# Kernel tuning notes

Hardware: AMD Instinct MI355X
Metric: run time of the kernel (lower is better)

The kernel has to match this reference:

```python
import jax, jax.numpy as jnp
import numpy as np

N, S, P, F = 128, 32, 16, 256   # agents, samples, processes, encoder dim
H, NH = 4, 128                  # heads, n_hidden (is_concat=False -> n_hidden=out_features)
SLOPE = 0.2


def setup_inputs() -> dict:
    key = jax.random.key(0)
    k1, k2, k3, k4 = jax.random.split(key, 4)
    h = jax.random.normal(k1, (N, S, P, F), dtype=jnp.float32)
    W_l = jax.random.normal(k2, (F, H * NH), dtype=jnp.float32) / np.float32(np.sqrt(F))
    W_r = jax.random.normal(k3, (F, H * NH), dtype=jnp.float32) / np.float32(np.sqrt(F))
    attn_w = jax.random.normal(k4, (2 * NH,), dtype=jnp.float32) / np.float32(np.sqrt(2 * NH))
    return {"h": h, "W_l": W_l, "W_r": W_r, "attn_w": attn_w}


def reference(h, W_l, W_r, attn_w):
    n, s, p, f = h.shape
    hp = jnp.transpose(h, (1, 2, 0, 3))                 # [S,P,N,F]
    g_l = (hp @ W_l).reshape(s, p, n, H, NH)            # [S,P,N,H,NH]
    g_r = (hp @ W_r).reshape(s, p, n, H, NH)
    # attn(concat(gl[j], gr[i])) == <gl[j], a_l> + <gr[i], a_r>
    a_l, a_r = attn_w[:NH], attn_w[NH:]
    score_l = jnp.einsum('spnhf,f->spnh', g_l, a_l)     # contributes along j
    score_r = jnp.einsum('spnhf,f->spnh', g_r, a_r)     # contributes along i
    e = score_r[:, :, :, None, :] + score_l[:, :, None, :, :]   # [S,P,i,j,H]
    e = jnp.where(e >= 0, e, SLOPE * e)                 # LeakyReLU
    diag = jnp.eye(n, dtype=bool)[None, None, :, :, None]
    e = jnp.where(diag, -jnp.inf, e)                    # mask self-attention
    a = jax.nn.softmax(e, axis=3)                       # softmax over j
    out = jnp.einsum('spijh,spjhf->spihf', a, g_r)      # [S,P,N,H,NH]
    out = out.mean(axis=3)                              # is_concat=False -> mean over heads
    out = jnp.transpose(out, (2, 0, 1, 3))              # [N,S,P,NH]
    return out, a
```

## Files before the change

### kernel.cpp

```cpp
#include <hip/hip_runtime.h>
#include <hip/hip_bf16.h>

#define DI __device__ __forceinline__

namespace {
constexpr int N_ = 128, S_ = 32, P_ = 16, F_ = 256, H_ = 4, NH_ = 128;
constexpr int SP_ = S_ * P_;
constexpr int ROWS_ = N_ * SP_;
constexpr int GC_ = H_ * NH_;
constexpr float SLOPE_ = 0.2f;
constexpr int OUT_ELEMS = N_ * SP_ * NH_;
}

DI float lrelu(float x) { return x >= 0.f ? x : SLOPE_ * x; }

DI unsigned short f2h(float x) {
    _Float16 h = (_Float16)x;
    return __builtin_bit_cast(unsigned short, h);
}
DI float h2f(unsigned short b) {
    return (float)__builtin_bit_cast(_Float16, b);
}

typedef _Float16 f16x8 __attribute__((ext_vector_type(8)));
typedef float    f32x4 __attribute__((ext_vector_type(4)));

DI f32x4 mfma16h(uint4 a, uint4 b, f32x4 c) {
    return __builtin_amdgcn_mfma_f32_16x16x32_f16(
        __builtin_bit_cast(f16x8, a), __builtin_bit_cast(f16x8, b), c, 0, 0, 0);
}

__global__ __launch_bounds__(256) void prep_kernel(
    const float* __restrict__ Wl, const float* __restrict__ Wr,
    const float* __restrict__ aw, float* __restrict__ wls, float* __restrict__ wrs) {
    int t = blockIdx.x * 256 + threadIdx.x;
    int which = t >> 10;
    int f = (t & 1023) >> 2;
    int h = t & 3;
    const float* W = which ? Wr : Wl;
    const float* a = aw + which * NH_;
    const float* wrow = W + (size_t)f * GC_ + h * NH_;
    float s = 0.f;
    for (int k = 0; k < NH_; ++k) s += wrow[k] * a[k];
    (which ? wrs : wls)[f * H_ + h] = s;
}

__global__ __launch_bounds__(256) void prep_bt(
    const float* __restrict__ Wr, unsigned short* __restrict__ bth,
    unsigned short* __restrict__ btl) {
    int t = blockIdx.x * 256 + threadIdx.x;
    int col = t >> 5, k0 = (t & 31) * 8;
    union { unsigned short us[8]; uint4 v; } ph, pl;
#pragma unroll
    for (int e = 0; e < 8; ++e) {
        float v = Wr[(size_t)(k0 + e) * GC_ + col] * 256.0f;
        unsigned short hi = f2h(v);
        ph.us[e] = hi;
        pl.us[e] = f2h(v - h2f(hi));
    }
    *(uint4*)&bth[col * F_ + k0] = ph.v;
    *(uint4*)&btl[col * F_ + k0] = pl.v;
}

__global__ __launch_bounds__(256) void score_kernel(
    const float* __restrict__ hm, const float* __restrict__ wls,
    const float* __restrict__ wrs, float* __restrict__ sl, float* __restrict__ sr) {
    int r = blockIdx.x * 256 + threadIdx.x;
    const float4* hr  = (const float4*)(hm + (size_t)r * F_);
    const float4* wl4 = (const float4*)wls;
    const float4* wr4 = (const float4*)wrs;
    float4 al = {0.f,0.f,0.f,0.f}, ar = {0.f,0.f,0.f,0.f};
    for (int f0 = 0; f0 < F_; f0 += 4) {
        float4 hv = hr[f0 >> 2];
        float hx[4] = {hv.x, hv.y, hv.z, hv.w};
#pragma unroll
        for (int u = 0; u < 4; ++u) {
            float4 wl = wl4[f0 + u], wr = wr4[f0 + u];
            al.x += hx[u] * wl.x; al.y += hx[u] * wl.y;
            al.z += hx[u] * wl.z; al.w += hx[u] * wl.w;
            ar.x += hx[u] * wr.x; ar.y += hx[u] * wr.y;
            ar.z += hx[u] * wr.z; ar.w += hx[u] * wr.w;
        }
    }
    int n = r >> 9, sp = r & 511;
    ((float4*)sl)[sp * N_ + n] = al;
    ((float4*)sr)[sp * N_ + n] = ar;
}

__global__ __launch_bounds__(512, 2) void gat_fused(
    const float* __restrict__ sl_g, const float* __restrict__ sr_g,
    const float* __restrict__ hm,
    const unsigned short* __restrict__ bth, const unsigned short* __restrict__ btl,
    float* __restrict__ a_out, float* __restrict__ out) {
    constexpr int PA = 40;
    __shared__ unsigned short Ah[2][128 * PA];
    __shared__ unsigned short Al[2][128 * PA];
    __shared__ unsigned short gt[128 * 128];
    __shared__ float4 sl4[N_], sr4[N_], mrow4[N_], invs4[N_];
    __shared__ float slh[H_][132];
    __shared__ float mx1[H_], mx2[H_];
    __shared__ int   id1[H_];

    int sp = blockIdx.x;
    int t = threadIdx.x;
    int w = t >> 6, l = t & 63;
    int ls = l & 15, kg = l >> 4;

    if (t < 128) {
        float4 v = ((const float4*)sl_g)[sp * N_ + t];
        sl4[t] = v;
        slh[0][t] = v.x; slh[1][t] = v.y; slh[2][t] = v.z; slh[3][t] = v.w;
    } else if (t < 256) {
        sr4[t - 128] = ((const float4*)sr_g)[sp * N_ + (t - 128)];
    }
    __syncthreads();

    if (t < H_) {
        float m1 = -1e30f; int i1 = 0;
        for (int j = 0; j < N_; ++j) {
            float v = ((const float*)&sl4[j])[t];
            if (v > m1) { m1 = v; i1 = j; }
        }
        float m2 = -1e30f;
        for (int j = 0; j < N_; ++j)
            if (j != i1) m2 = fmaxf(m2, ((const float*)&sl4[j])[t]);
        mx1[t] = m1; mx2[t] = m2; id1[t] = i1;
    }
    __syncthreads();

    int arow = t >> 2, akc = (t & 3) * 8;
    const float* abase = hm + ((size_t)arow * 512 + sp) * 256 + akc;
    float4 s0 = *(const float4*)(abase);
    float4 s1 = *(const float4*)(abase + 4);

    {
        int i = t & 127, h = t >> 7;
        float sri = ((const float*)&sr4[i])[h];
        float m = lrelu(sri + ((id1[h] == i) ? mx2[h] : mx1[h]));
        float sum = 0.f;
        for (int j = 0; j < N_; ++j) {
            float e = lrelu(sri + ((const float*)&sl4[j])[h]);
            float p = __expf(e - m);
            if (j != i) sum += p;
        }
        ((float*)&mrow4[i])[h] = m;
        ((float*)&invs4[i])[h] = 1.f / sum;
    }

    {
        float av[8] = {s0.x, s0.y, s0.z, s0.w, s1.x, s1.y, s1.z, s1.w};
        union { unsigned short us[8]; uint4 v; } ph, pl;
#pragma unroll
        for (int e = 0; e < 8; ++e) {
            unsigned short hi = f2h(av[e]);
            ph.us[e] = hi;
            pl.us[e] = f2h(av[e] - h2f(hi));
        }
        *(uint4*)&Ah[0][arow * PA + akc] = ph.v;
        *(uint4*)&Al[0][arow * PA + akc] = pl.v;
    }
    __syncthreads();

    f32x4 acc[8][4];
#pragma unroll
    for (int m = 0; m < 8; ++m)
#pragma unroll
        for (int n = 0; n < 4; ++n) acc[m][n] = (f32x4){0.f, 0.f, 0.f, 0.f};

    float4* a_base_g = (float4*)(a_out + (size_t)sp * 65536);
    int aj = t & 127, ib = t >> 7;
    float4 slv = sl4[aj];

    for (int step = 0; step < 8; ++step) {
        int cur = step & 1;
        float4 n0, n1;
        if (step < 7) {
            n0 = *(const float4*)(abase + (step + 1) * 32);
            n1 = *(const float4*)(abase + (step + 1) * 32 + 4);
        }
        int kglob = step * 32 + kg * 8;
        uint4 fbh[4], fbl[4];
#pragma unroll
        for (int n = 0; n < 4; ++n) {
            int c = n * 128 + w * 16 + ls;
            fbh[n] = *(const uint4*)&bth[(size_t)c * F_ + kglob];
            fbl[n] = *(const uint4*)&btl[(size_t)c * F_ + kglob];
        }
#pragma unroll
        for (int q = 0; q < 4; ++q) {
            int i = step * 16 + q * 4 + ib;
            float4 srv = sr4[i], m4 = mrow4[i], s4 = invs4[i];
            float4 p;
            p.x = __expf(lrelu(srv.x + slv.x) - m4.x) * s4.x;
            p.y = __expf(lrelu(srv.y + slv.y) - m4.y) * s4.y;
            p.z = __expf(lrelu(srv.z + slv.z) - m4.z) * s4.z;
            p.w = __expf(lrelu(srv.w + slv.w) - m4.w) * s4.w;
            if (aj == i) { p.x = 0.f; p.y = 0.f; p.z = 0.f; p.w = 0.f; }
            a_base_g[i * N_ + aj] = p;
        }
#pragma unroll
        for (int m = 0; m < 8; ++m) {
            int row = m * 16 + ls;
            uint4 fah = *(const uint4*)&Ah[cur][row * PA + kg * 8];
            uint4 fal = *(const uint4*)&Al[cur][row * PA + kg * 8];
#pragma unroll
            for (int n = 0; n < 4; ++n) {
                acc[m][n] = mfma16h(fah, fbh[n], acc[m][n]);
                acc[m][n] = mfma16h(fah, fbl[n], acc[m][n]);
                acc[m][n] = mfma16h(fal, fbh[n], acc[m][n]);
            }
        }
        if (step < 7) {
            float av[8] = {n0.x, n0.y, n0.z, n0.w, n1.x, n1.y, n1.z, n1.w};
            union { unsigned short us[8]; uint4 v; } ph, pl;
#pragma unroll
            for (int e = 0; e < 8; ++e) {
                unsigned short hi = f2h(av[e]);
                ph.us[e] = hi;
                pl.us[e] = f2h(av[e] - h2f(hi));
            }
            *(uint4*)&Ah[cur ^ 1][arow * PA + akc] = ph.v;
            *(uint4*)&Al[cur ^ 1][arow * PA + akc] = pl.v;
        }
        __syncthreads();
    }

    f32x4 aco[8];
#pragma unroll
    for (int n = 0; n < 8; ++n) aco[n] = (f32x4){0.f, 0.f, 0.f, 0.f};

    int i_my = w * 16 + ls;
    int fl   = w * 16 + ls;
    int swz  = (ls & 7) << 3;

    for (int h = 0; h < H_; ++h) {
        if (h) __syncthreads();

#pragma unroll
        for (int m = 0; m < 8; ++m) {
            int nodeb = m * 16 + kg * 4;
            union { unsigned short us[4]; uint2 v; } pk;
#pragma unroll
            for (int q = 0; q < 4; ++q) pk.us[q] = f2h(acc[m][h][q] * 0.00390625f);
            *(uint2*)&gt[fl * 128 + (nodeb ^ swz)] = pk.v;
        }
        __syncthreads();

        float sri = ((const float*)&sr4[i_my])[h];
        float mh  = ((const float*)&mrow4[i_my])[h];
        float sh  = ((const float*)&invs4[i_my])[h];
        uint4 pa[4];
#pragma unroll
        for (int k0i = 0; k0i < 4; ++k0i) {
            int jb = k0i * 32 + kg * 8;
            union { unsigned short us[8]; uint4 v; } pk;
#pragma unroll
            for (int e = 0; e < 8; ++e) {
                int j = jb + e;
                float p = (j == i_my) ? 0.f
                        : __expf(lrelu(sri + slh[h][j]) - mh) * sh;
                pk.us[e] = f2h(p);
            }
            pa[k0i] = pk.v;
        }
#pragma unroll
        for (int k0i = 0; k0i < 4; ++k0i) {
            int koff = k0i * 32 + kg * 8;
#pragma unroll
            for (int n = 0; n < 8; ++n) {
                int f = n * 16 + ls;
                uint4 fb = *(const uint4*)&gt[f * 128 + (koff ^ swz)];
                aco[n] = mfma16h(pa[k0i], fb, aco[n]);
            }
        }
    }

#pragma unroll
    for (int n = 0; n < 8; ++n) {
        int f = n * 16 + ls;
#pragma unroll
        for (int q = 0; q < 4; ++q)
            out[(size_t)(w * 16 + kg * 4 + q) * 65536 + (size_t)sp * NH_ + f] =
                aco[n][q] * 0.25f;
    }
}

extern "C" void kernel_launch(void* const* d_in, const int* in_sizes, int n_in,
                              void* d_out, int out_size, void* d_ws, size_t ws_size,
                              hipStream_t stream) {
    const float* hm = (const float*)d_in[0];
    const float* Wl = (const float*)d_in[1];
    const float* Wr = (const float*)d_in[2];
    const float* aw = (const float*)d_in[3];

    float* out   = (float*)d_out;
    float* a_out = out + OUT_ELEMS;

    char* ws = (char*)d_ws;
    float* sl  = (float*)ws;
    float* sr  = sl + SP_ * N_ * H_;
    float* wls = sr + SP_ * N_ * H_;
    float* wrs = wls + F_ * H_;
    unsigned short* bth = (unsigned short*)(wrs + F_ * H_);
    unsigned short* btl = bth + GC_ * F_;

    prep_kernel <<<8,           256, 0, stream>>>(Wl, Wr, aw, wls, wrs);
    prep_bt     <<<64,          256, 0, stream>>>(Wr, bth, btl);
    score_kernel<<<ROWS_ / 256, 256, 0, stream>>>(hm, wls, wrs, sl, sr);
    gat_fused   <<<SP_,         512, 0, stream>>>(sl, sr, hm, bth, btl, a_out, out);
}
```

Baseline: 150.3 us.

## Overlap softmax stats with GEMM steps and stage all heads in shared memory

Spreads the per-row softmax denominator loop across the first four GEMM k-steps and writes the attention matrix during the last four, instead of computing both up front. The top-2 max search is split into a parallel partial reduction. Packed cvt_pkrtz conversions replace per-element half conversion, and all four heads of g are written to one aliased 128KB shared buffer at once, which removes per-head barriers. s_setprio is raised around the second MFMA loop. The larger shared allocation (about 141KB) may reduce occupancy from the two blocks per CU requested by the launch bounds, and round-toward-zero conversion changes rounding slightly.

```diff
diff --git a/kernel.cpp b/kernel.cpp
--- a/kernel.cpp
+++ b/kernel.cpp
@@ -22,8 +22,14 @@
     return (float)__builtin_bit_cast(_Float16, b);
 }
 
+typedef __fp16   fp16x2 __attribute__((ext_vector_type(2)));
 typedef _Float16 f16x8 __attribute__((ext_vector_type(8)));
 typedef float    f32x4 __attribute__((ext_vector_type(4)));
+
+DI unsigned int pk2(float a, float b) {
+    fp16x2 r = __builtin_amdgcn_cvt_pkrtz(a, b);
+    return __builtin_bit_cast(unsigned int, r);
+}
 
 DI f32x4 mfma16h(uint4 a, uint4 b, f32x4 c) {
     return __builtin_amdgcn_mfma_f32_16x16x32_f16(
@@ -93,13 +99,23 @@
     const unsigned short* __restrict__ bth, const unsigned short* __restrict__ btl,
     float* __restrict__ a_out, float* __restrict__ out) {
     constexpr int PA = 40;
-    __shared__ unsigned short Ah[2][128 * PA];
-    __shared__ unsigned short Al[2][128 * PA];
-    __shared__ unsigned short gt[128 * 128];
-    __shared__ float4 sl4[N_], sr4[N_], mrow4[N_], invs4[N_];
-    __shared__ float slh[H_][132];
-    __shared__ float mx1[H_], mx2[H_];
-    __shared__ int   id1[H_];
+    __shared__ __align__(16) unsigned char SMEM[141440];
+    unsigned short* Ah0 = (unsigned short*)SMEM;
+    unsigned short* Ah1 = Ah0 + 128 * PA;
+    unsigned short* Al0 = Ah1 + 128 * PA;
+    unsigned short* Al1 = Al0 + 128 * PA;
+    unsigned short* gt4 = (unsigned short*)SMEM;
+    float4* sl4   = (float4*)(SMEM + 131072);
+    float4* sr4   = (float4*)(SMEM + 133120);
+    float4* mrow4 = (float4*)(SMEM + 135168);
+    float4* invs4 = (float4*)(SMEM + 137216);
+    float*  slh   = (float*)(SMEM + 139264);
+    float*  mx1   = (float*)(SMEM + 141376);
+    float*  mx2   = (float*)(SMEM + 141392);
+    int*    id1   = (int*)(SMEM + 141408);
+    float* pm1 = (float*)mrow4;
+    float* pm2 = pm1 + 128;
+    int*   pid = (int*)(pm2 + 128);
 
     int sp = blockIdx.x;
     int t = threadIdx.x;
@@ -109,22 +125,10 @@
     if (t < 128) {
         float4 v = ((const float4*)sl_g)[sp * N_ + t];
         sl4[t] = v;
-        slh[0][t] = v.x; slh[1][t] = v.y; slh[2][t] = v.z; slh[3][t] = v.w;
+        slh[0 * 132 + t] = v.x; slh[1 * 132 + t] = v.y;
+        slh[2 * 132 + t] = v.z; slh[3 * 132 + t] = v.w;
     } else if (t < 256) {
         sr4[t - 128] = ((const float4*)sr_g)[sp * N_ + (t - 128)];
-    }
-    __syncthreads();
-
-    if (t < H_) {
-        float m1 = -1e30f; int i1 = 0;
-        for (int j = 0; j < N_; ++j) {
-            float v = ((const float*)&sl4[j])[t];
-            if (v > m1) { m1 = v; i1 = j; }
-        }
-        float m2 = -1e30f;
-        for (int j = 0; j < N_; ++j)
-            if (j != i1) m2 = fmaxf(m2, ((const float*)&sl4[j])[t]);
-        mx1[t] = m1; mx2[t] = m2; id1[t] = i1;
     }
     __syncthreads();
 
@@ -133,32 +137,52 @@
     float4 s0 = *(const float4*)(abase);
     float4 s1 = *(const float4*)(abase + 4);
 
-    {
-        int i = t & 127, h = t >> 7;
-        float sri = ((const float*)&sr4[i])[h];
-        float m = lrelu(sri + ((id1[h] == i) ? mx2[h] : mx1[h]));
-        float sum = 0.f;
-        for (int j = 0; j < N_; ++j) {
-            float e = lrelu(sri + ((const float*)&sl4[j])[h]);
-            float p = __expf(e - m);
-            if (j != i) sum += p;
-        }
-        ((float*)&mrow4[i])[h] = m;
-        ((float*)&invs4[i])[h] = 1.f / sum;
-    }
+    if (t < 128) {
+        int h = t >> 5, seg = t & 31;
+        float m1 = -1e30f, m2 = -1e30f; int i1 = -1;
+#pragma unroll
+        for (int jj = 0; jj < 4; ++jj) {
+            int j = seg * 4 + jj;
+            float v = slh[h * 132 + j];
+            if (v > m1) { m2 = m1; m1 = v; i1 = j; }
+            else m2 = fmaxf(m2, v);
+        }
+        pm1[h * 32 + seg] = m1; pm2[h * 32 + seg] = m2; pid[h * 32 + seg] = i1;
+    }
+    __syncthreads();
+    if (t < H_) {
+        float m1 = -1e30f, m2 = -1e30f; int i1 = -1;
+        for (int s = 0; s < 32; ++s) {
+            float a1 = pm1[t * 32 + s], a2 = pm2[t * 32 + s]; int ai = pid[t * 32 + s];
+            if (a1 > m1) { m2 = fmaxf(m1, a2); m1 = a1; i1 = ai; }
+            else m2 = fmaxf(m2, a1);
+        }
+        mx1[t] = m1; mx2[t] = m2; id1[t] = i1;
+    }
+    __syncthreads();
 
     {
         float av[8] = {s0.x, s0.y, s0.z, s0.w, s1.x, s1.y, s1.z, s1.w};
-        union { unsigned short us[8]; uint4 v; } ph, pl;
-#pragma unroll
-        for (int e = 0; e < 8; ++e) {
-            unsigned short hi = f2h(av[e]);
-            ph.us[e] = hi;
-            pl.us[e] = f2h(av[e] - h2f(hi));
-        }
-        *(uint4*)&Ah[0][arow * PA + akc] = ph.v;
-        *(uint4*)&Al[0][arow * PA + akc] = pl.v;
-    }
+        uint4 vh, vl;
+        unsigned int* ph = (unsigned int*)&vh;
+        unsigned int* pl = (unsigned int*)&vl;
+#pragma unroll
+        for (int e = 0; e < 8; e += 2) {
+            unsigned int hp = pk2(av[e], av[e + 1]);
+            float r0 = av[e]     - h2f((unsigned short)(hp & 0xffff));
+            float r1 = av[e + 1] - h2f((unsigned short)(hp >> 16));
+            ph[e >> 1] = hp;
+            pl[e >> 1] = pk2(r0, r1);
+        }
+        *(uint4*)&Ah0[arow * PA + akc] = vh;
+        *(uint4*)&Al0[arow * PA + akc] = vl;
+    }
+
+    int p1i = t & 127, p1h = t >> 7;
+    float p1sri = ((const float*)&sr4[p1i])[p1h];
+    float p1m = lrelu(p1sri + ((id1[p1h] == p1i) ? mx2[p1h] : mx1[p1h]));
+    float p1sum = 0.f;
+
     __syncthreads();
 
     f32x4 acc[8][4];
@@ -172,7 +196,10 @@
     float4 slv = sl4[aj];
 
     for (int step = 0; step < 8; ++step) {
-        int cur = step & 1;
+        unsigned short* AhC = (step & 1) ? Ah1 : Ah0;
+        unsigned short* AlC = (step & 1) ? Al1 : Al0;
+        unsigned short* AhN = (step & 1) ? Ah0 : Ah1;
+        unsigned short* AlN = (step & 1) ? Al0 : Al1;
         float4 n0, n1;
         if (step < 7) {
             n0 = *(const float4*)(abase + (step + 1) * 32);
@@ -186,23 +213,38 @@
             fbh[n] = *(const uint4*)&bth[(size_t)c * F_ + kglob];
             fbl[n] = *(const uint4*)&btl[(size_t)c * F_ + kglob];
         }
-#pragma unroll
-        for (int q = 0; q < 4; ++q) {
-            int i = step * 16 + q * 4 + ib;
-            float4 srv = sr4[i], m4 = mrow4[i], s4 = invs4[i];
-            float4 p;
-            p.x = __expf(lrelu(srv.x + slv.x) - m4.x) * s4.x;
-            p.y = __expf(lrelu(srv.y + slv.y) - m4.y) * s4.y;
-            p.z = __expf(lrelu(srv.z + slv.z) - m4.z) * s4.z;
-            p.w = __expf(lrelu(srv.w + slv.w) - m4.w) * s4.w;
-            if (aj == i) { p.x = 0.f; p.y = 0.f; p.z = 0.f; p.w = 0.f; }
-            a_base_g[i * N_ + aj] = p;
+        if (step < 4) {
+            int j0 = step * 32;
+#pragma unroll 4
+            for (int j = j0; j < j0 + 32; ++j) {
+                float e = lrelu(p1sri + slh[p1h * 132 + j]);
+                float p = __expf(e - p1m);
+                if (j != p1i) p1sum += p;
+            }
+            if (step == 3) {
+                ((float*)&mrow4[p1i])[p1h] = p1m;
+                ((float*)&invs4[p1i])[p1h] = 1.f / p1sum;
+            }
+        } else {
+            int ibase2 = (step - 4) * 32;
+#pragma unroll
+            for (int q = 0; q < 8; ++q) {
+                int i = ibase2 + q * 4 + ib;
+                float4 srv = sr4[i], m4 = mrow4[i], s4 = invs4[i];
+                float4 p;
+                p.x = __expf(lrelu(srv.x + slv.x) - m4.x) * s4.x;
+                p.y = __expf(lrelu(srv.y + slv.y) - m4.y) * s4.y;
+                p.z = __expf(lrelu(srv.z + slv.z) - m4.z) * s4.z;
+                p.w = __expf(lrelu(srv.w + slv.w) - m4.w) * s4.w;
+                if (aj == i) { p.x = 0.f; p.y = 0.f; p.z = 0.f; p.w = 0.f; }
+                a_base_g[i * N_ + aj] = p;
+            }
         }
 #pragma unroll
         for (int m = 0; m < 8; ++m) {
             int row = m * 16 + ls;
-            uint4 fah = *(const uint4*)&Ah[cur][row * PA + kg * 8];
-            uint4 fal = *(const uint4*)&Al[cur][row * PA + kg * 8];
+            uint4 fah = *(const uint4*)&AhC[row * PA + kg * 8];
+            uint4 fal = *(const uint4*)&AlC[row * PA + kg * 8];
 #pragma unroll
             for (int n = 0; n < 4; ++n) {
                 acc[m][n] = mfma16h(fah, fbh[n], acc[m][n]);
@@ -212,40 +254,45 @@
         }
         if (step < 7) {
             float av[8] = {n0.x, n0.y, n0.z, n0.w, n1.x, n1.y, n1.z, n1.w};
-            union { unsigned short us[8]; uint4 v; } ph, pl;
-#pragma unroll
-            for (int e = 0; e < 8; ++e) {
-                unsigned short hi = f2h(av[e]);
-                ph.us[e] = hi;
-                pl.us[e] = f2h(av[e] - h2f(hi));
-            }
-            *(uint4*)&Ah[cur ^ 1][arow * PA + akc] = ph.v;
-            *(uint4*)&Al[cur ^ 1][arow * PA + akc] = pl.v;
+            uint4 vh, vl;
+            unsigned int* ph = (unsigned int*)&vh;
+            unsigned int* pl = (unsigned int*)&vl;
+#pragma unroll
+            for (int e = 0; e < 8; e += 2) {
+                unsigned int hp = pk2(av[e], av[e + 1]);
+                float r0 = av[e]     - h2f((unsigned short)(hp & 0xffff));
+                float r1 = av[e + 1] - h2f((unsigned short)(hp >> 16));
+                ph[e >> 1] = hp;
+                pl[e >> 1] = pk2(r0, r1);
+            }
+            *(uint4*)&AhN[arow * PA + akc] = vh;
+            *(uint4*)&AlN[arow * PA + akc] = vl;
         }
         __syncthreads();
     }
 
+    int fl  = w * 16 + ls;
+    int swz = (ls & 7) << 3;
+    constexpr float gs = 0.00390625f;
+#pragma unroll
+    for (int m = 0; m < 8; ++m) {
+        int nx = (m * 16 + kg * 4) ^ swz;
+#pragma unroll
+        for (int h = 0; h < H_; ++h) {
+            uint2 pk;
+            pk.x = pk2(acc[m][h][0] * gs, acc[m][h][1] * gs);
+            pk.y = pk2(acc[m][h][2] * gs, acc[m][h][3] * gs);
+            *(uint2*)&gt4[h * 16384 + fl * 128 + nx] = pk;
+        }
+    }
+    __syncthreads();
+
     f32x4 aco[8];
 #pragma unroll
     for (int n = 0; n < 8; ++n) aco[n] = (f32x4){0.f, 0.f, 0.f, 0.f};
 
     int i_my = w * 16 + ls;
-    int fl   = w * 16 + ls;
-    int swz  = (ls & 7) << 3;
-
     for (int h = 0; h < H_; ++h) {
-        if (h) __syncthreads();
-
-#pragma unroll
-        for (int m = 0; m < 8; ++m) {
-            int nodeb = m * 16 + kg * 4;
-            union { unsigned short us[4]; uint2 v; } pk;
-#pragma unroll
-            for (int q = 0; q < 4; ++q) pk.us[q] = f2h(acc[m][h][q] * 0.00390625f);
-            *(uint2*)&gt[fl * 128 + (nodeb ^ swz)] = pk.v;
-        }
-        __syncthreads();
-
         float sri = ((const float*)&sr4[i_my])[h];
         float mh  = ((const float*)&mrow4[i_my])[h];
         float sh  = ((const float*)&invs4[i_my])[h];
@@ -258,21 +305,23 @@
             for (int e = 0; e < 8; ++e) {
                 int j = jb + e;
                 float p = (j == i_my) ? 0.f
-                        : __expf(lrelu(sri + slh[h][j]) - mh) * sh;
+                        : __expf(lrelu(sri + slh[h * 132 + j]) - mh) * sh;
                 pk.us[e] = f2h(p);
             }
             pa[k0i] = pk.v;
         }
+        __builtin_amdgcn_s_setprio(1);
 #pragma unroll
         for (int k0i = 0; k0i < 4; ++k0i) {
             int koff = k0i * 32 + kg * 8;
 #pragma unroll
             for (int n = 0; n < 8; ++n) {
                 int f = n * 16 + ls;
-                uint4 fb = *(const uint4*)&gt[f * 128 + (koff ^ swz)];
+                uint4 fb = *(const uint4*)&gt4[h * 16384 + f * 128 + (koff ^ swz)];
                 aco[n] = mfma16h(pa[k0i], fb, aco[n]);
             }
         }
+        __builtin_amdgcn_s_setprio(0);
     }
 
 #pragma unroll
```

New measurement: 140.4 us. 6.6% less time.
